# Kernel optimization log

Hardware: AMD Instinct MI355X
Metric: run time of the kernel (lower is better)

## Reference

```python
import jax, jax.numpy as jnp
import numpy as np

B, H, W = 64, 84, 84
IN_F, HID, NCLS = 128, 256, 50
C2 = IN_F * 2  # 256
EPS = 1e-5
K_NEIGH = 4


def _ring_edges(batch):
    rows = np.repeat(np.arange(batch), K_NEIGH)
    offs = np.tile(np.arange(1, K_NEIGH + 1), batch)
    cols = (rows + offs) % batch
    return jnp.asarray(np.stack([rows, cols]), dtype=jnp.int32)


def setup_inputs() -> dict:
    key = jax.random.key(0)
    ks = jax.random.split(key, 40)
    i = iter(range(40))
    def n(shape, s=0.05):
        return jax.random.normal(ks[next(i)], shape, jnp.float32) * s
    def u(shape):
        return jax.random.uniform(ks[next(i)], shape, jnp.float32, 0.5, 1.5)
    d = {}
    d['x'] = jax.random.normal(ks[next(i)], (B, 3, H, W), jnp.float32)
    # conv1 + bn1
    d['conv1_w'] = n((IN_F, 3, 3, 3)); d['conv1_b'] = n((IN_F,))
    d['bn1_g'] = 1.0 + n((IN_F,)); d['bn1_b'] = n((IN_F,))
    d['bn1_m'] = n((IN_F,)); d['bn1_v'] = u((IN_F,))
    # conv2 + bn2
    d['conv2_w'] = n((C2, IN_F, 3, 3)); d['conv2_b'] = n((C2,))
    d['bn2_g'] = 1.0 + n((C2,)); d['bn2_b'] = n((C2,))
    d['bn2_m'] = n((C2,)); d['bn2_v'] = u((C2,))
    # conv3 + bn3
    d['conv3_w'] = n((C2, C2, 3, 3)); d['conv3_b'] = n((C2,))
    d['bn3_g'] = 1.0 + n((C2,)); d['bn3_b'] = n((C2,))
    d['bn3_m'] = n((C2,)); d['bn3_v'] = u((C2,))
    # gcn1: Linear(256,256), attn Linear(512,1)
    d['gcn1_lw'] = n((HID, C2)); d['gcn1_lb'] = n((HID,))
    d['gcn1_aw'] = n((1, 2 * C2)); d['gcn1_ab'] = n((1,))
    # gcn2: Linear(256,256), attn Linear(512,1)
    d['gcn2_lw'] = n((HID, HID)); d['gcn2_lb'] = n((HID,))
    d['gcn2_aw'] = n((1, 2 * HID)); d['gcn2_ab'] = n((1,))
    # fc
    d['fc_w'] = n((NCLS, HID)); d['fc_b'] = n((NCLS,))
    d['edge_index'] = _ring_edges(B)  # [2, 4*B] deterministic ring graph
    return d


def _conv_bn_relu(x, w, b, g, be, m, v):
    y = jax.lax.conv_general_dilated(
        x, w, window_strides=(1, 1), padding='SAME',
        dimension_numbers=('NCHW', 'OIHW', 'NCHW')) + b[None, :, None, None]
    scale = (g / jnp.sqrt(v + EPS))[None, :, None, None]
    y = (y - m[None, :, None, None]) * scale + be[None, :, None, None]
    return jax.nn.relu(y)


def _gcn_conv(h, row, col, lw, lb, aw, ab):
    # h: [N, F]; edge gather -> attn MLP -> global softmax -> scatter-add
    ef = jnp.concatenate([h[row], h[col]], axis=1)          # [E, 2F]
    ew = jax.nn.leaky_relu(ef @ aw.T + ab, 0.01)            # [E, 1]
    ew = jax.nn.softmax(ew, axis=0)                          # softmax over all edges
    agg = jnp.zeros_like(h).at[row].add(h[col] * ew)        # [N, F]
    return agg @ lw.T + lb + h                               # linear + residual


def reference(x, conv1_w, conv1_b, bn1_g, bn1_b, bn1_m, bn1_v,
              conv2_w, conv2_b, bn2_g, bn2_b, bn2_m, bn2_v,
              conv3_w, conv3_b, bn3_g, bn3_b, bn3_m, bn3_v,
              gcn1_lw, gcn1_lb, gcn1_aw, gcn1_ab,
              gcn2_lw, gcn2_lb, gcn2_aw, gcn2_ab,
              fc_w, fc_b, edge_index):
    h = _conv_bn_relu(x, conv1_w, conv1_b, bn1_g, bn1_b, bn1_m, bn1_v)
    h = _conv_bn_relu(h, conv2_w, conv2_b, bn2_g, bn2_b, bn2_m, bn2_v)
    h = _conv_bn_relu(h, conv3_w, conv3_b, bn3_g, bn3_b, bn3_m, bn3_v)
    h = h.mean(axis=(2, 3))                                  # adaptive avg pool 1x1 + flatten -> [B, 256]
    row, col = edge_index[0], edge_index[1]
    h = jax.nn.relu(_gcn_conv(h, row, col, gcn1_lw, gcn1_lb, gcn1_aw, gcn1_ab))
    h = jax.nn.relu(_gcn_conv(h, row, col, gcn2_lw, gcn2_lb, gcn2_aw, gcn2_ab))
    return h @ fc_w.T + fc_b                                 # [B, 50]
```

## Files before the change

### kernel.cpp

```cpp
#include <hip/hip_runtime.h>
#include <hip/hip_bf16.h>

typedef __attribute__((ext_vector_type(8))) short bf16x8;
typedef __attribute__((ext_vector_type(4))) float f32x4;

#define DEV __device__ __forceinline__

static constexpr int Bn   = 64;
static constexpr int Hs   = 84;
static constexpr int HP   = 86;
static constexpr int C1c  = 128;
static constexpr int C2c  = 256;
static constexpr int NPOS = Hs * Hs;
static constexpr float EPSf = 1e-5f;

DEV __hip_bfloat16 f2b(float v) { return __float2bfloat16(v); }

DEV void gload16(const void* g, void* l) {
    __builtin_amdgcn_global_load_lds(
        (const __attribute__((address_space(1))) void*)g,
        (__attribute__((address_space(3))) void*)l, 16, 0, 0);
}

__global__ __launch_bounds__(128) void conv1_k(
    const float* __restrict__ x,
    const float* __restrict__ w,  const float* __restrict__ cb,
    const float* __restrict__ g,  const float* __restrict__ be,
    const float* __restrict__ mm, const float* __restrict__ vv,
    __hip_bfloat16* __restrict__ h1)
{
    __shared__ float xin[3][3][HP];
    int bi = blockIdx.x;
    int b = bi / Hs, y = bi % Hs;
    int t = threadIdx.x;

    for (int idx = t; idx < 3 * 3 * HP; idx += 128) {
        int ci = idx / (3 * HP);
        int r  = idx % (3 * HP);
        int dy = r / HP;
        int xx = r % HP;
        int iy = y + dy - 1;
        int ix = xx - 1;
        float v = 0.f;
        if (iy >= 0 && iy < Hs && ix >= 0 && ix < Hs)
            v = x[((size_t)(b * 3 + ci) * Hs + iy) * Hs + ix];
        xin[ci][dy][xx] = v;
    }
    int co = t;
    float wr[3][3][3];
    for (int ci = 0; ci < 3; ci++)
        for (int dy = 0; dy < 3; dy++)
            for (int dx = 0; dx < 3; dx++)
                wr[ci][dy][dx] = w[((co * 3 + ci) * 3 + dy) * 3 + dx];
    float scale = g[co] / sqrtf(vv[co] + EPSf);
    float bias  = (cb[co] - mm[co]) * scale + be[co];
    __syncthreads();

    for (int xp = 0; xp < Hs; xp++) {
        float acc = 0.f;
        #pragma unroll
        for (int ci = 0; ci < 3; ci++)
            #pragma unroll
            for (int dy = 0; dy < 3; dy++)
                #pragma unroll
                for (int dx = 0; dx < 3; dx++)
                    acc += xin[ci][dy][xp + dx] * wr[ci][dy][dx];
        float o = acc * scale + bias;
        o = o > 0.f ? o : 0.f;
        h1[((size_t)(b * HP + y + 1) * HP + (xp + 1)) * C1c + co] = f2b(o);
    }
}

template <int C>
__global__ void halo_zero(__hip_bfloat16* __restrict__ h)
{
    int i = blockIdx.x;
    int b = i / 340, p = i % 340;
    int y, xx;
    if (p < 86)       { y = 0;  xx = p; }
    else if (p < 172) { y = 85; xx = p - 86; }
    else if (p < 256) { xx = 0; y = p - 172 + 1; }
    else              { xx = 85; y = p - 256 + 1; }
    h[((size_t)(b * HP + y) * HP + xx) * C + threadIdx.x] = f2b(0.f);
}

template <int CIN>
__global__ void prep_w(const float* __restrict__ w, __hip_bfloat16* __restrict__ wm)
{
    int e  = blockIdx.x * 256 + threadIdx.x;
    int k  = e >> 8;
    int co = e & 255;
    int tap = k / CIN;
    int ci  = k % CIN;
    int ty = tap / 3, tx = tap % 3;
    wm[(size_t)(k >> 5) * 8192 + co * 32 + (k & 31)] =
        f2b(w[((size_t)(co * CIN + ci) * 3 + ty) * 3 + tx]);
}

__global__ void prep_sb(const float* __restrict__ cb, const float* __restrict__ g,
                        const float* __restrict__ be, const float* __restrict__ mm,
                        const float* __restrict__ vv, float* __restrict__ sb)
{
    int co = threadIdx.x;
    float s = g[co] / sqrtf(vv[co] + EPSf);
    sb[co] = s;
    sb[256 + co] = (cb[co] - mm[co]) * s + be[co];
}

__global__ void zero_f32(float* __restrict__ p)
{
    p[blockIdx.x * 256 + threadIdx.x] = 0.f;
}

template <int CIN, bool POOL>
__global__ __launch_bounds__(256) void conv_igemm(
    const __hip_bfloat16* __restrict__ in, const __hip_bfloat16* __restrict__ wm,
    const float* __restrict__ sb, __hip_bfloat16* __restrict__ out, float* __restrict__ pool)
{
    constexpr int KB = CIN / 32;
    __shared__ __align__(16) unsigned short As[128 * 32];
    __shared__ __align__(16) unsigned short Bs[128 * 32];
    __shared__ float pl[256];

    int t = threadIdx.x;
    int l = t & 63, w = t >> 6;
    int lidx = l & 15, lg = l >> 4;
    int wr = w >> 1, wc = w & 1;

    int nwg  = (int)gridDim.x;
    int orig = (int)blockIdx.x;
    int xcd = orig & 7, idx = orig >> 3;
    int q = nwg >> 3, r = nwg & 7;
    int bx = (xcd < r ? xcd * (q + 1) : r * (q + 1) + (xcd - r) * q) + idx;

    int mtile = bx >> 1, nhalf = bx & 1;
    int m0 = mtile * 128;
    int n0 = nhalf * 128;

    int srow = w * 32 + (l >> 2);
    int sseg = l & 3;
    int gmA0 = m0 + srow;
    int gmA1 = m0 + srow + 16;
    int bA0 = gmA0 / NPOS; int rA0 = gmA0 - bA0 * NPOS; int yA0 = rA0 / Hs; int xA0 = rA0 - yA0 * Hs;
    int bA1 = gmA1 / NPOS; int rA1 = gmA1 - bA1 * NPOS; int yA1 = rA1 / Hs; int xA1 = rA1 - yA1 * Hs;
    const __hip_bfloat16* aBase0 = in + ((size_t)(bA0 * HP + yA0) * HP + xA0) * CIN + sseg * 8;
    const __hip_bfloat16* aBase1 = in + ((size_t)(bA1 * HP + yA1) * HP + xA1) * CIN + sseg * 8;
    const __hip_bfloat16* bBase0 = wm + (size_t)(n0 + srow) * 32 + sseg * 8;
    const __hip_bfloat16* bBase1 = wm + (size_t)(n0 + srow + 16) * 32 + sseg * 8;
    char* aDst0 = (char*)As + (w * 32 +  0) * 64;
    char* aDst1 = (char*)As + (w * 32 + 16) * 64;
    char* bDst0 = (char*)Bs + (w * 32 +  0) * 64;
    char* bDst1 = (char*)Bs + (w * 32 + 16) * 64;

    f32x4 acc[4][4];
    #pragma unroll
    for (int i = 0; i < 4; i++)
        #pragma unroll
        for (int j = 0; j < 4; j++)
            acc[i][j] = (f32x4){0.f, 0.f, 0.f, 0.f};
    if (POOL) pl[t] = 0.f;

    for (int kb = 0; kb < KB; kb++) {
        size_t koff = (size_t)kb * 32;
        #pragma unroll
        for (int tap = 0; tap < 9; tap++) {
            int ty = tap / 3, tx = tap - ty * 3;
            size_t aoff = (size_t)(ty * HP + tx) * CIN + koff;
            size_t boff = (size_t)(tap * KB + kb) * 8192;
            gload16(aBase0 + aoff, aDst0);
            gload16(aBase1 + aoff, aDst1);
            gload16(bBase0 + boff, bDst0);
            gload16(bBase1 + boff, bDst1);
            __syncthreads();
            bf16x8 av[4], bv[4];
            #pragma unroll
            for (int m = 0; m < 4; m++)
                av[m] = *(const bf16x8*)&As[(wr * 64 + m * 16 + lidx) * 32 + lg * 8];
            #pragma unroll
            for (int n = 0; n < 4; n++)
                bv[n] = *(const bf16x8*)&Bs[(wc * 64 + n * 16 + lidx) * 32 + lg * 8];
            #pragma unroll
            for (int m = 0; m < 4; m++)
                #pragma unroll
                for (int n = 0; n < 4; n++)
                    acc[m][n] = __builtin_amdgcn_mfma_f32_16x16x32_bf16(av[m], bv[n], acc[m][n], 0, 0, 0);
            __syncthreads();
        }
    }

    float sc[4], bi2[4];
    #pragma unroll
    for (int n = 0; n < 4; n++) {
        int cn = n0 + wc * 64 + n * 16 + lidx;
        sc[n]  = sb[cn];
        bi2[n] = sb[256 + cn];
    }

    if (!POOL) {
        #pragma unroll
        for (int m = 0; m < 4; m++) {
            #pragma unroll
            for (int r2 = 0; r2 < 4; r2++) {
                int row = wr * 64 + m * 16 + lg * 4 + r2;
                int gm2 = m0 + row;
                int b2  = gm2 / NPOS;
                int rm2 = gm2 - b2 * NPOS;
                int y2  = rm2 / Hs;
                int x2  = rm2 - y2 * Hs;
                size_t ob = ((size_t)(b2 * HP + y2 + 1) * HP + (x2 + 1)) * 256;
                #pragma unroll
                for (int n = 0; n < 4; n++) {
                    float v = acc[m][n][r2] * sc[n] + bi2[n];
                    v = v > 0.f ? v : 0.f;
                    out[ob + n0 + wc * 64 + n * 16 + lidx] = f2b(v);
                }
            }
        }
    } else {
        int bs_lo   = m0 / NPOS;
        int row_lim = (bs_lo + 1) * NPOS - m0;
        #pragma unroll
        for (int n = 0; n < 4; n++) {
            float s0 = 0.f, s1 = 0.f;
            #pragma unroll
            for (int m = 0; m < 4; m++)
                #pragma unroll
                for (int r2 = 0; r2 < 4; r2++) {
                    int row = wr * 64 + m * 16 + lg * 4 + r2;
                    float v = acc[m][n][r2] * sc[n] + bi2[n];
                    v = v > 0.f ? v : 0.f;
                    if (row < row_lim) s0 += v; else s1 += v;
                }
            int cl = wc * 64 + n * 16 + lidx;
            atomicAdd(&pl[cl], s0);
            if (row_lim < 128) atomicAdd(&pl[128 + cl], s1);
        }
        __syncthreads();
        if (t < 128)
            atomicAdd(&pool[bs_lo * 256 + n0 + t], pl[t]);
        else if (row_lim < 128)
            atomicAdd(&pool[(bs_lo + 1) * 256 + n0 + (t - 128)], pl[t]);
    }
}

__global__ void pool_div(const float* __restrict__ pool, float* __restrict__ h0)
{
    int i = blockIdx.x * 256 + threadIdx.x;
    h0[i] = pool[i] * (1.0f / (float)NPOS);
}

__global__ __launch_bounds__(256) void gcn_attn(
    const float* __restrict__ h, const float* __restrict__ aw,
    const float* __restrict__ ab, const int* __restrict__ ei,
    float* __restrict__ ew)
{
    __shared__ float p[64], q[64], red[256];
    int t = threadIdx.x;
    if (t < 64) {
        float pp = 0.f, qq = 0.f;
        for (int c = 0; c < 256; c++) {
            float hv = h[t * 256 + c];
            pp += hv * aw[c];
            qq += hv * aw[256 + c];
        }
        p[t] = pp; q[t] = qq;
    }
    __syncthreads();
    int r = ei[t], c = ei[256 + t];
    float s = p[r] + q[c] + ab[0];
    s = s >= 0.f ? s : 0.01f * s;
    red[t] = s;
    __syncthreads();
    for (int st = 128; st > 0; st >>= 1) {
        if (t < st) red[t] = fmaxf(red[t], red[t + st]);
        __syncthreads();
    }
    float mx = red[0];
    __syncthreads();
    float e = expf(s - mx);
    red[t] = e;
    __syncthreads();
    for (int st = 128; st > 0; st >>= 1) {
        if (t < st) red[t] += red[t + st];
        __syncthreads();
    }
    ew[t] = e / red[0];
}

__global__ __launch_bounds__(256) void gcn_agg(
    const float* __restrict__ h, const float* __restrict__ ew, const int* __restrict__ ei,
    const float* __restrict__ lw, const float* __restrict__ lb,
    float* __restrict__ ho)
{
    __shared__ float agg[256];
    __shared__ float ewl[256];
    __shared__ int rl[256], cl[256];
    int n = blockIdx.x;
    int t = threadIdx.x;
    ewl[t] = ew[t];
    rl[t] = ei[t];
    cl[t] = ei[256 + t];
    __syncthreads();
    float a = 0.f;
    for (int e = 0; e < 256; e++)
        if (rl[e] == n) a += ewl[e] * h[cl[e] * 256 + t];
    agg[t] = a;
    __syncthreads();
    float o = 0.f;
    for (int c2 = 0; c2 < 256; c2++)
        o += agg[c2] * lw[t * 256 + c2];
    o += lb[t] + h[n * 256 + t];
    o = o > 0.f ? o : 0.f;
    ho[n * 256 + t] = o;
}

__global__ void fc_k(const float* __restrict__ h, const float* __restrict__ fw,
                     const float* __restrict__ fb, float* __restrict__ out)
{
    int n = blockIdx.x;
    int t = threadIdx.x;
    if (t < 50) {
        float o = 0.f;
        for (int c = 0; c < 256; c++)
            o += h[n * 256 + c] * fw[t * 256 + c];
        o += fb[t];
        out[n * 50 + t] = o;
    }
}

extern "C" void kernel_launch(void* const* d_in, const int* in_sizes, int n_in,
                              void* d_out, int out_size, void* d_ws, size_t ws_size,
                              hipStream_t stream)
{
    (void)in_sizes; (void)n_in; (void)out_size;

    const float* X    = (const float*)d_in[0];
    const float* c1w  = (const float*)d_in[1];
    const float* c1b  = (const float*)d_in[2];
    const float* b1g  = (const float*)d_in[3];
    const float* b1b  = (const float*)d_in[4];
    const float* b1m  = (const float*)d_in[5];
    const float* b1v  = (const float*)d_in[6];
    const float* c2w  = (const float*)d_in[7];
    const float* c2b  = (const float*)d_in[8];
    const float* b2g  = (const float*)d_in[9];
    const float* b2b  = (const float*)d_in[10];
    const float* b2m  = (const float*)d_in[11];
    const float* b2v  = (const float*)d_in[12];
    const float* c3w  = (const float*)d_in[13];
    const float* c3b  = (const float*)d_in[14];
    const float* b3g  = (const float*)d_in[15];
    const float* b3b  = (const float*)d_in[16];
    const float* b3m  = (const float*)d_in[17];
    const float* b3v  = (const float*)d_in[18];
    const float* g1lw = (const float*)d_in[19];
    const float* g1lb = (const float*)d_in[20];
    const float* g1aw = (const float*)d_in[21];
    const float* g1ab = (const float*)d_in[22];
    const float* g2lw = (const float*)d_in[23];
    const float* g2lb = (const float*)d_in[24];
    const float* g2aw = (const float*)d_in[25];
    const float* g2ab = (const float*)d_in[26];
    const float* fcw  = (const float*)d_in[27];
    const float* fcb  = (const float*)d_in[28];
    const int*   EI   = (const int*)d_in[29];

    size_t fixedB = 3000000;
    int chb = 8;
    if (ws_size >= (size_t)64 * 5680128 + fixedB)      chb = 64;
    else if (ws_size >= (size_t)32 * 5680128 + fixedB) chb = 32;
    else if (ws_size >= (size_t)16 * 5680128 + fixedB) chb = 16;
    int nchunks = Bn / chb;
    int mch = chb * NPOS;

    char* p = (char*)d_ws;
    auto carve = [&](size_t bytes) {
        char* r = p;
        p += (bytes + 255) & ~(size_t)255;
        return r;
    };
    __hip_bfloat16* h1c = (__hip_bfloat16*)carve((size_t)chb * HP * HP * C1c * 2);
    __hip_bfloat16* h2c = (__hip_bfloat16*)carve((size_t)chb * HP * HP * C2c * 2);
    __hip_bfloat16* wm2 = (__hip_bfloat16*)carve((size_t)9 * C1c * 256 * 2);
    __hip_bfloat16* wm3 = (__hip_bfloat16*)carve((size_t)9 * C2c * 256 * 2);
    float* sb2  = (float*)carve(512 * 4);
    float* sb3  = (float*)carve(512 * 4);
    float* pool = (float*)carve(64 * 256 * 4);
    float* h0   = (float*)carve(64 * 256 * 4);
    float* hg1  = (float*)carve(64 * 256 * 4);
    float* hg2  = (float*)carve(64 * 256 * 4);
    float* ew1  = (float*)carve(256 * 4);
    float* ew2  = (float*)carve(256 * 4);

    halo_zero<C1c><<<dim3(chb * 340), dim3(C1c), 0, stream>>>(h1c);
    halo_zero<C2c><<<dim3(chb * 340), dim3(C2c), 0, stream>>>(h2c);
    prep_w<C1c><<<dim3(9 * C1c), dim3(256), 0, stream>>>(c2w, wm2);
    prep_w<C2c><<<dim3(9 * C2c), dim3(256), 0, stream>>>(c3w, wm3);
    prep_sb<<<dim3(1), dim3(256), 0, stream>>>(c2b, b2g, b2b, b2m, b2v, sb2);
    prep_sb<<<dim3(1), dim3(256), 0, stream>>>(c3b, b3g, b3b, b3m, b3v, sb3);
    zero_f32<<<dim3(64), dim3(256), 0, stream>>>(pool);

    for (int ch = 0; ch < nchunks; ch++) {
        const float* xch = X + (size_t)ch * chb * 3 * NPOS;
        conv1_k<<<dim3(chb * Hs), dim3(C1c), 0, stream>>>(
            xch, c1w, c1b, b1g, b1b, b1m, b1v, h1c);
        conv_igemm<C1c, false><<<dim3((mch / 128) * 2), dim3(256), 0, stream>>>(
            h1c, wm2, sb2, h2c, nullptr);
        conv_igemm<C2c, true ><<<dim3((mch / 128) * 2), dim3(256), 0, stream>>>(
            h2c, wm3, sb3, nullptr, pool + (size_t)ch * chb * 256);
    }
    pool_div<<<dim3(64), dim3(256), 0, stream>>>(pool, h0);

    gcn_attn<<<dim3(1), dim3(256), 0, stream>>>(h0, g1aw, g1ab, EI, ew1);
    gcn_agg<<<dim3(64), dim3(256), 0, stream>>>(h0, ew1, EI, g1lw, g1lb, hg1);
    gcn_attn<<<dim3(1), dim3(256), 0, stream>>>(hg1, g2aw, g2ab, EI, ew2);
    gcn_agg<<<dim3(64), dim3(256), 0, stream>>>(hg1, ew2, EI, g2lw, g2lb, hg2);
    fc_k<<<dim3(64), dim3(64), 0, stream>>>(hg2, fcw, fcb, (float*)d_out);
}
```

Baseline: 989.3 us.

## Triple-buffer implicit-GEMM conv with full-N tiles and swizzled LDS

Reworks the conv implicit-GEMM kernel so each block computes a 128x256 output tile, covering all output channels, instead of 128x128, which halves the grid. The K loop becomes a three-stage LDS ring that issues global-to-LDS loads two steps ahead and waits with partial vmcnt, replacing the per-step double syncthreads. LDS rows get an XOR swizzle to reduce bank conflicts, and MFMA sections run with raised priority. The wider tile doubles accumulator registers and LDS use, with launch_bounds(256,2), which may limit occupancy.

```diff
diff --git a/kernel.cpp b/kernel.cpp
--- a/kernel.cpp
+++ b/kernel.cpp
@@ -113,85 +113,114 @@
 }
 
 template <int CIN, bool POOL>
-__global__ __launch_bounds__(256) void conv_igemm(
-    const __hip_bfloat16* __restrict__ in, const __hip_bfloat16* __restrict__ wm,
+__global__ __launch_bounds__(256, 2) void conv_igemm(
+    const __hip_bfloat16* __restrict__ in, const __hip_bfloat16* __restrict__ wgt,
     const float* __restrict__ sb, __hip_bfloat16* __restrict__ out, float* __restrict__ pool)
 {
     constexpr int KB = CIN / 32;
-    __shared__ __align__(16) unsigned short As[128 * 32];
-    __shared__ __align__(16) unsigned short Bs[128 * 32];
-    __shared__ float pl[256];
+    constexpr int NT = 9 * KB;
+    __shared__ __align__(16) unsigned short As[3 * 128 * 32];
+    __shared__ __align__(16) unsigned short Bs[3 * 256 * 32];
+    __shared__ float pl[512];
 
     int t = threadIdx.x;
     int l = t & 63, w = t >> 6;
     int lidx = l & 15, lg = l >> 4;
-    int wr = w >> 1, wc = w & 1;
+    int wm = w >> 1, wn = w & 1;
 
     int nwg  = (int)gridDim.x;
     int orig = (int)blockIdx.x;
     int xcd = orig & 7, idx = orig >> 3;
     int q = nwg >> 3, r = nwg & 7;
     int bx = (xcd < r ? xcd * (q + 1) : r * (q + 1) + (xcd - r) * q) + idx;
-
-    int mtile = bx >> 1, nhalf = bx & 1;
-    int m0 = mtile * 128;
-    int n0 = nhalf * 128;
-
-    int srow = w * 32 + (l >> 2);
-    int sseg = l & 3;
-    int gmA0 = m0 + srow;
-    int gmA1 = m0 + srow + 16;
-    int bA0 = gmA0 / NPOS; int rA0 = gmA0 - bA0 * NPOS; int yA0 = rA0 / Hs; int xA0 = rA0 - yA0 * Hs;
-    int bA1 = gmA1 / NPOS; int rA1 = gmA1 - bA1 * NPOS; int yA1 = rA1 / Hs; int xA1 = rA1 - yA1 * Hs;
-    const __hip_bfloat16* aBase0 = in + ((size_t)(bA0 * HP + yA0) * HP + xA0) * CIN + sseg * 8;
-    const __hip_bfloat16* aBase1 = in + ((size_t)(bA1 * HP + yA1) * HP + xA1) * CIN + sseg * 8;
-    const __hip_bfloat16* bBase0 = wm + (size_t)(n0 + srow) * 32 + sseg * 8;
-    const __hip_bfloat16* bBase1 = wm + (size_t)(n0 + srow + 16) * 32 + sseg * 8;
-    char* aDst0 = (char*)As + (w * 32 +  0) * 64;
-    char* aDst1 = (char*)As + (w * 32 + 16) * 64;
-    char* bDst0 = (char*)Bs + (w * 32 +  0) * 64;
-    char* bDst1 = (char*)Bs + (w * 32 + 16) * 64;
-
-    f32x4 acc[4][4];
+    int m0 = bx * 128;
+
+    int sseg = (l & 3) ^ ((l >> 3) & 3);
+    int srow = w * 16 + (l >> 2);
+    const __hip_bfloat16 *pA0, *pA1, *pB0, *pB1, *pB2, *pB3;
+    {
+        int gm0 = m0 + srow;
+        int b0 = gm0 / NPOS; int r0 = gm0 - b0 * NPOS; int y0 = r0 / Hs; int x0 = r0 - y0 * Hs;
+        pA0 = in + ((size_t)(b0 * HP + y0) * HP + x0) * CIN + sseg * 8;
+        int gm1 = m0 + srow + 64;
+        int b1 = gm1 / NPOS; int r1 = gm1 - b1 * NPOS; int y1 = r1 / Hs; int x1 = r1 - y1 * Hs;
+        pA1 = in + ((size_t)(b1 * HP + y1) * HP + x1) * CIN + sseg * 8;
+        pB0 = wgt + (size_t)(srow      ) * 32 + sseg * 8;
+        pB1 = wgt + (size_t)(srow +  64) * 32 + sseg * 8;
+        pB2 = wgt + (size_t)(srow + 128) * 32 + sseg * 8;
+        pB3 = wgt + (size_t)(srow + 192) * 32 + sseg * 8;
+    }
+    char* AsB = (char*)As;
+    char* BsB = (char*)Bs;
+
+    int swz = (lidx >> 1) & 3;
+    unsigned aLane = (unsigned)((wm * 64  + lidx) * 64 + ((lg ^ swz) * 16));
+    unsigned bLane = (unsigned)((wn * 128 + lidx) * 64 + ((lg ^ swz) * 16));
+
+    f32x4 acc[4][8];
     #pragma unroll
-    for (int i = 0; i < 4; i++)
-        #pragma unroll
-        for (int j = 0; j < 4; j++)
-            acc[i][j] = (f32x4){0.f, 0.f, 0.f, 0.f};
-    if (POOL) pl[t] = 0.f;
-
-    for (int kb = 0; kb < KB; kb++) {
-        size_t koff = (size_t)kb * 32;
-        #pragma unroll
-        for (int tap = 0; tap < 9; tap++) {
-            int ty = tap / 3, tx = tap - ty * 3;
-            size_t aoff = (size_t)(ty * HP + tx) * CIN + koff;
-            size_t boff = (size_t)(tap * KB + kb) * 8192;
-            gload16(aBase0 + aoff, aDst0);
-            gload16(aBase1 + aoff, aDst1);
-            gload16(bBase0 + boff, bDst0);
-            gload16(bBase1 + boff, bDst1);
-            __syncthreads();
-            bf16x8 av[4], bv[4];
+    for (int m = 0; m < 4; m++)
+        #pragma unroll
+        for (int n = 0; n < 8; n++)
+            acc[m][n] = (f32x4){0.f, 0.f, 0.f, 0.f};
+    if (POOL) { pl[t] = 0.f; pl[256 + t] = 0.f; }
+
+    auto ISSUE = [&](int k, unsigned cA, unsigned cB) {
+        int tap = k / KB, kb = k - tap * KB;
+        int ty = tap / 3, tx = tap - ty * 3;
+        size_t aoff = (size_t)(ty * HP + tx) * CIN + kb * 32;
+        size_t boff = (size_t)k * 8192;
+        gload16(pA0 + aoff, AsB + cA + w * 1024);
+        gload16(pA1 + aoff, AsB + cA + w * 1024 + 4096);
+        gload16(pB0 + boff, BsB + cB + w * 1024);
+        gload16(pB1 + boff, BsB + cB + w * 1024 + 4096);
+        gload16(pB2 + boff, BsB + cB + w * 1024 + 8192);
+        gload16(pB3 + boff, BsB + cB + w * 1024 + 12288);
+    };
+
+    auto COMP = [&](unsigned cA, unsigned cB) {
+        bf16x8 av[4]; bf16x8 bv[8];
+        #pragma unroll
+        for (int m = 0; m < 4; m++)
+            av[m] = *(const bf16x8*)(AsB + cA + aLane + m * 1024);
+        #pragma unroll
+        for (int n = 0; n < 8; n++)
+            bv[n] = *(const bf16x8*)(BsB + cB + bLane + n * 1024);
+        __builtin_amdgcn_s_setprio(1);
+        #pragma unroll
+        for (int m = 0; m < 4; m++)
             #pragma unroll
-            for (int m = 0; m < 4; m++)
-                av[m] = *(const bf16x8*)&As[(wr * 64 + m * 16 + lidx) * 32 + lg * 8];
-            #pragma unroll
-            for (int n = 0; n < 4; n++)
-                bv[n] = *(const bf16x8*)&Bs[(wc * 64 + n * 16 + lidx) * 32 + lg * 8];
-            #pragma unroll
-            for (int m = 0; m < 4; m++)
-                #pragma unroll
-                for (int n = 0; n < 4; n++)
-                    acc[m][n] = __builtin_amdgcn_mfma_f32_16x16x32_bf16(av[m], bv[n], acc[m][n], 0, 0, 0);
-            __syncthreads();
-        }
-    }
-
-    float sc[4], bi2[4];
+            for (int n = 0; n < 8; n++)
+                acc[m][n] = __builtin_amdgcn_mfma_f32_16x16x32_bf16(av[m], bv[n], acc[m][n], 0, 0, 0);
+        __builtin_amdgcn_s_setprio(0);
+    };
+
+    ISSUE(0, 0u, 0u);
+    ISSUE(1, 8192u, 16384u);
+
+    unsigned cA0 = 0u,     cB0 = 0u;
+    unsigned cA1 = 8192u,  cB1 = 16384u;
+    unsigned cA2 = 16384u, cB2 = 32768u;
+    for (int kt = 0; kt < NT - 1; ++kt) {
+        asm volatile("s_waitcnt vmcnt(6) lgkmcnt(0)" ::: "memory");
+        __builtin_amdgcn_s_barrier();
+        asm volatile("" ::: "memory");
+        if (kt + 2 < NT) ISSUE(kt + 2, cA2, cB2);
+        COMP(cA0, cB0);
+        unsigned ta = cA0, tb = cB0;
+        cA0 = cA1; cB0 = cB1;
+        cA1 = cA2; cB1 = cB2;
+        cA2 = ta;  cB2 = tb;
+    }
+    asm volatile("s_waitcnt vmcnt(0) lgkmcnt(0)" ::: "memory");
+    __builtin_amdgcn_s_barrier();
+    asm volatile("" ::: "memory");
+    COMP(cA0, cB0);
+
+    float sc[8], bi2[8];
     #pragma unroll
-    for (int n = 0; n < 4; n++) {
-        int cn = n0 + wc * 64 + n * 16 + lidx;
+    for (int n = 0; n < 8; n++) {
+        int cn = wn * 128 + n * 16 + lidx;
         sc[n]  = sb[cn];
         bi2[n] = sb[256 + cn];
     }
@@ -201,7 +230,7 @@
         for (int m = 0; m < 4; m++) {
             #pragma unroll
             for (int r2 = 0; r2 < 4; r2++) {
-                int row = wr * 64 + m * 16 + lg * 4 + r2;
+                int row = wm * 64 + m * 16 + lg * 4 + r2;
                 int gm2 = m0 + row;
                 int b2  = gm2 / NPOS;
                 int rm2 = gm2 - b2 * NPOS;
@@ -209,10 +238,10 @@
                 int x2  = rm2 - y2 * Hs;
                 size_t ob = ((size_t)(b2 * HP + y2 + 1) * HP + (x2 + 1)) * 256;
                 #pragma unroll
-                for (int n = 0; n < 4; n++) {
+                for (int n = 0; n < 8; n++) {
                     float v = acc[m][n][r2] * sc[n] + bi2[n];
                     v = v > 0.f ? v : 0.f;
-                    out[ob + n0 + wc * 64 + n * 16 + lidx] = f2b(v);
+                    out[ob + wn * 128 + n * 16 + lidx] = f2b(v);
                 }
             }
         }
@@ -220,26 +249,24 @@
         int bs_lo   = m0 / NPOS;
         int row_lim = (bs_lo + 1) * NPOS - m0;
         #pragma unroll
-        for (int n = 0; n < 4; n++) {
+        for (int n = 0; n < 8; n++) {
             float s0 = 0.f, s1 = 0.f;
             #pragma unroll
             for (int m = 0; m < 4; m++)
                 #pragma unroll
                 for (int r2 = 0; r2 < 4; r2++) {
-                    int row = wr * 64 + m * 16 + lg * 4 + r2;
+                    int row = wm * 64 + m * 16 + lg * 4 + r2;
                     float v = acc[m][n][r2] * sc[n] + bi2[n];
                     v = v > 0.f ? v : 0.f;
                     if (row < row_lim) s0 += v; else s1 += v;
                 }
-            int cl = wc * 64 + n * 16 + lidx;
+            int cl = wn * 128 + n * 16 + lidx;
             atomicAdd(&pl[cl], s0);
-            if (row_lim < 128) atomicAdd(&pl[128 + cl], s1);
+            if (row_lim < 128) atomicAdd(&pl[256 + cl], s1);
         }
         __syncthreads();
-        if (t < 128)
-            atomicAdd(&pool[bs_lo * 256 + n0 + t], pl[t]);
-        else if (row_lim < 128)
-            atomicAdd(&pool[(bs_lo + 1) * 256 + n0 + (t - 128)], pl[t]);
+        atomicAdd(&pool[bs_lo * 256 + t], pl[t]);
+        if (row_lim < 128) atomicAdd(&pool[(bs_lo + 1) * 256 + t], pl[256 + t]);
     }
 }
 
@@ -404,9 +431,9 @@
         const float* xch = X + (size_t)ch * chb * 3 * NPOS;
         conv1_k<<<dim3(chb * Hs), dim3(C1c), 0, stream>>>(
             xch, c1w, c1b, b1g, b1b, b1m, b1v, h1c);
-        conv_igemm<C1c, false><<<dim3((mch / 128) * 2), dim3(256), 0, stream>>>(
+        conv_igemm<C1c, false><<<dim3(mch / 128), dim3(256), 0, stream>>>(
             h1c, wm2, sb2, h2c, nullptr);
-        conv_igemm<C2c, true ><<<dim3((mch / 128) * 2), dim3(256), 0, stream>>>(
+        conv_igemm<C2c, true ><<<dim3(mch / 128), dim3(256), 0, stream>>>(
             h2c, wm3, sb3, nullptr, pool + (size_t)ch * chb * 256);
     }
     pool_div<<<dim3(64), dim3(256), 0, stream>>>(pool, h0);
```

Measured after the change: 1.045 ms. +5.7%, slower.

## Pipeline conv implicit-GEMM with triple-buffered LDS and a 128x256 tile

Applied to the files above, without the earlier changes.

Rewrites the conv2/conv3 implicit-GEMM main loop. Each block now has 512 threads and covers all 256 output channels for 128 pixels, which removes the duplicated A loads of the old two N-halves. Each iteration processes two K-steps, with async global-to-LDS loads issued two iterations ahead into a three-way rotating buffer. The loop uses split B fragment loads, explicit vmcnt/lgkmcnt waits, s_barrier, and setprio around the MFMA bursts. The aim is to hide global load latency and cut per-tap barrier overhead. The cost is a large LDS footprint (about 147 KB), which limits occupancy to one block per CU, plus fragile hand-written wait counts.

```diff
diff --git a/kernel.cpp b/kernel.cpp
--- a/kernel.cpp
+++ b/kernel.cpp
@@ -113,44 +113,50 @@
 }
 
 template <int CIN, bool POOL>
-__global__ __launch_bounds__(256) void conv_igemm(
-    const __hip_bfloat16* __restrict__ in, const __hip_bfloat16* __restrict__ wm,
+__global__ __launch_bounds__(512, 2) void conv_igemm(
+    const __hip_bfloat16* __restrict__ in, const __hip_bfloat16* __restrict__ wgt,
     const float* __restrict__ sb, __hip_bfloat16* __restrict__ out, float* __restrict__ pool)
 {
     constexpr int KB = CIN / 32;
-    __shared__ __align__(16) unsigned short As[128 * 32];
-    __shared__ __align__(16) unsigned short Bs[128 * 32];
-    __shared__ float pl[256];
+    constexpr int NK = 9 * KB / 2;
+    constexpr unsigned BUF = 49152u;
+    __shared__ __align__(16) char lds[3 * 49152];
+    __shared__ float pl[512];
 
     int t = threadIdx.x;
     int l = t & 63, w = t >> 6;
     int lidx = l & 15, lg = l >> 4;
-    int wr = w >> 1, wc = w & 1;
+    int wm = w >> 2, wn = w & 3;
 
     int nwg  = (int)gridDim.x;
     int orig = (int)blockIdx.x;
     int xcd = orig & 7, idx = orig >> 3;
     int q = nwg >> 3, r = nwg & 7;
     int bx = (xcd < r ? xcd * (q + 1) : r * (q + 1) + (xcd - r) * q) + idx;
-
-    int mtile = bx >> 1, nhalf = bx & 1;
-    int m0 = mtile * 128;
-    int n0 = nhalf * 128;
-
-    int srow = w * 32 + (l >> 2);
-    int sseg = l & 3;
-    int gmA0 = m0 + srow;
-    int gmA1 = m0 + srow + 16;
-    int bA0 = gmA0 / NPOS; int rA0 = gmA0 - bA0 * NPOS; int yA0 = rA0 / Hs; int xA0 = rA0 - yA0 * Hs;
-    int bA1 = gmA1 / NPOS; int rA1 = gmA1 - bA1 * NPOS; int yA1 = rA1 / Hs; int xA1 = rA1 - yA1 * Hs;
-    const __hip_bfloat16* aBase0 = in + ((size_t)(bA0 * HP + yA0) * HP + xA0) * CIN + sseg * 8;
-    const __hip_bfloat16* aBase1 = in + ((size_t)(bA1 * HP + yA1) * HP + xA1) * CIN + sseg * 8;
-    const __hip_bfloat16* bBase0 = wm + (size_t)(n0 + srow) * 32 + sseg * 8;
-    const __hip_bfloat16* bBase1 = wm + (size_t)(n0 + srow + 16) * 32 + sseg * 8;
-    char* aDst0 = (char*)As + (w * 32 +  0) * 64;
-    char* aDst1 = (char*)As + (w * 32 + 16) * 64;
-    char* bDst0 = (char*)Bs + (w * 32 +  0) * 64;
-    char* bDst1 = (char*)Bs + (w * 32 + 16) * 64;
+    int m0 = bx * 128;
+
+    int seg  = t & 3;
+    int srow = t >> 2;
+    const __hip_bfloat16* pA;
+    {
+        int gm = m0 + srow;
+        int b0 = gm / NPOS; int r0 = gm - b0 * NPOS;
+        int y0 = r0 / Hs;   int x0 = r0 - y0 * Hs;
+        pA = in + ((size_t)(b0 * HP + y0) * HP + x0) * CIN + seg * 8;
+    }
+    const __hip_bfloat16* pB = wgt + (size_t)srow * 32 + seg * 8;
+
+    unsigned aRd[4][2], bRd[4][2];
+    #pragma unroll
+    for (int mf = 0; mf < 4; mf++)
+        #pragma unroll
+        for (int kh = 0; kh < 2; kh++)
+            aRd[mf][kh] = (unsigned)(kh * 8192 + (wm * 64 + mf * 16 + lidx) * 64 + lg * 16);
+    #pragma unroll
+    for (int nf = 0; nf < 4; nf++)
+        #pragma unroll
+        for (int kh = 0; kh < 2; kh++)
+            bRd[nf][kh] = (unsigned)(16384 + kh * 16384 + (wn * 64 + nf * 16 + lidx) * 64 + lg * 16);
 
     f32x4 acc[4][4];
     #pragma unroll
@@ -160,48 +166,103 @@
             acc[i][j] = (f32x4){0.f, 0.f, 0.f, 0.f};
     if (POOL) pl[t] = 0.f;
 
-    for (int kb = 0; kb < KB; kb++) {
-        size_t koff = (size_t)kb * 32;
-        #pragma unroll
-        for (int tap = 0; tap < 9; tap++) {
-            int ty = tap / 3, tx = tap - ty * 3;
-            size_t aoff = (size_t)(ty * HP + tx) * CIN + koff;
-            size_t boff = (size_t)(tap * KB + kb) * 8192;
-            gload16(aBase0 + aoff, aDst0);
-            gload16(aBase1 + aoff, aDst1);
-            gload16(bBase0 + boff, bDst0);
-            gload16(bBase1 + boff, bDst1);
-            __syncthreads();
-            bf16x8 av[4], bv[4];
-            #pragma unroll
-            for (int m = 0; m < 4; m++)
-                av[m] = *(const bf16x8*)&As[(wr * 64 + m * 16 + lidx) * 32 + lg * 8];
-            #pragma unroll
-            for (int n = 0; n < 4; n++)
-                bv[n] = *(const bf16x8*)&Bs[(wc * 64 + n * 16 + lidx) * 32 + lg * 8];
-            #pragma unroll
-            for (int m = 0; m < 4; m++)
+    auto AOFF = [&](int s) -> size_t {
+        int kb = s / 9, tap = s - kb * 9;
+        int ty = tap / 3, tx = tap - ty * 3;
+        return (size_t)(ty * HP + tx) * CIN + kb * 32;
+    };
+    auto BOFF = [&](int s) -> size_t {
+        int kb = s / 9, tap = s - kb * 9;
+        return (size_t)(tap * KB + kb) * 8192;
+    };
+    auto ISSUE_P0 = [&](int kt2, unsigned nb) {
+        int s0 = 2 * kt2, s1 = s0 + 1;
+        gload16(pA + AOFF(s0), lds + nb +          w * 1024);
+        gload16(pA + AOFF(s1), lds + nb +  8192 + w * 1024);
+        gload16(pB + BOFF(s0), lds + nb + 16384 + w * 1024);
+    };
+    auto ISSUE_P1 = [&](int kt2, unsigned nb) {
+        int s0 = 2 * kt2, s1 = s0 + 1;
+        gload16(pB + BOFF(s0) + 4096, lds + nb + 24576 + w * 1024);
+        gload16(pB + BOFF(s1),        lds + nb + 32768 + w * 1024);
+        gload16(pB + BOFF(s1) + 4096, lds + nb + 40960 + w * 1024);
+    };
+
+    ISSUE_P0(0, 0u); ISSUE_P1(0, 0u);
+    ISSUE_P0(1, BUF); ISSUE_P1(1, BUF);
+
+    for (int kt = 0; kt < NK; ++kt) {
+        unsigned cb = (unsigned)(kt % 3) * BUF;
+        unsigned nb = (unsigned)((kt + 2) % 3) * BUF;
+        bool more = (kt + 2) < NK;
+
+        if (kt + 1 < NK) asm volatile("s_waitcnt vmcnt(6)" ::: "memory");
+        else             asm volatile("s_waitcnt vmcnt(0)" ::: "memory");
+        __builtin_amdgcn_s_barrier();
+
+        bf16x8 av[4][2], bv0[2][2];
+        #pragma unroll
+        for (int mf = 0; mf < 4; mf++)
+            #pragma unroll
+            for (int kh = 0; kh < 2; kh++)
+                av[mf][kh] = *(const bf16x8*)(lds + cb + aRd[mf][kh]);
+        #pragma unroll
+        for (int nf = 0; nf < 2; nf++)
+            #pragma unroll
+            for (int kh = 0; kh < 2; kh++)
+                bv0[nf][kh] = *(const bf16x8*)(lds + cb + bRd[nf][kh]);
+        if (more) ISSUE_P0(kt + 2, nb);
+        __builtin_amdgcn_s_barrier();
+        asm volatile("s_waitcnt lgkmcnt(0)" ::: "memory");
+        __builtin_amdgcn_sched_barrier(0);
+        __builtin_amdgcn_s_setprio(1);
+        #pragma unroll
+        for (int kh = 0; kh < 2; kh++)
+            #pragma unroll
+            for (int mf = 0; mf < 4; mf++)
                 #pragma unroll
-                for (int n = 0; n < 4; n++)
-                    acc[m][n] = __builtin_amdgcn_mfma_f32_16x16x32_bf16(av[m], bv[n], acc[m][n], 0, 0, 0);
-            __syncthreads();
-        }
+                for (int nf = 0; nf < 2; nf++)
+                    acc[mf][nf] = __builtin_amdgcn_mfma_f32_16x16x32_bf16(
+                        av[mf][kh], bv0[nf][kh], acc[mf][nf], 0, 0, 0);
+        __builtin_amdgcn_s_setprio(0);
+
+        __builtin_amdgcn_s_barrier();
+        bf16x8 bv1[2][2];
+        #pragma unroll
+        for (int nf = 0; nf < 2; nf++)
+            #pragma unroll
+            for (int kh = 0; kh < 2; kh++)
+                bv1[nf][kh] = *(const bf16x8*)(lds + cb + bRd[2 + nf][kh]);
+        if (more) ISSUE_P1(kt + 2, nb);
+        __builtin_amdgcn_s_barrier();
+        asm volatile("s_waitcnt lgkmcnt(0)" ::: "memory");
+        __builtin_amdgcn_sched_barrier(0);
+        __builtin_amdgcn_s_setprio(1);
+        #pragma unroll
+        for (int kh = 0; kh < 2; kh++)
+            #pragma unroll
+            for (int mf = 0; mf < 4; mf++)
+                #pragma unroll
+                for (int nf = 0; nf < 2; nf++)
+                    acc[mf][2 + nf] = __builtin_amdgcn_mfma_f32_16x16x32_bf16(
+                        av[mf][kh], bv1[nf][kh], acc[mf][2 + nf], 0, 0, 0);
+        __builtin_amdgcn_s_setprio(0);
     }
 
     float sc[4], bi2[4];
     #pragma unroll
-    for (int n = 0; n < 4; n++) {
-        int cn = n0 + wc * 64 + n * 16 + lidx;
-        sc[n]  = sb[cn];
-        bi2[n] = sb[256 + cn];
+    for (int nf = 0; nf < 4; nf++) {
+        int cn = wn * 64 + nf * 16 + lidx;
+        sc[nf]  = sb[cn];
+        bi2[nf] = sb[256 + cn];
     }
 
     if (!POOL) {
         #pragma unroll
-        for (int m = 0; m < 4; m++) {
+        for (int mf = 0; mf < 4; mf++) {
             #pragma unroll
             for (int r2 = 0; r2 < 4; r2++) {
-                int row = wr * 64 + m * 16 + lg * 4 + r2;
+                int row = wm * 64 + mf * 16 + lg * 4 + r2;
                 int gm2 = m0 + row;
                 int b2  = gm2 / NPOS;
                 int rm2 = gm2 - b2 * NPOS;
@@ -209,37 +270,38 @@
                 int x2  = rm2 - y2 * Hs;
                 size_t ob = ((size_t)(b2 * HP + y2 + 1) * HP + (x2 + 1)) * 256;
                 #pragma unroll
-                for (int n = 0; n < 4; n++) {
-                    float v = acc[m][n][r2] * sc[n] + bi2[n];
+                for (int nf = 0; nf < 4; nf++) {
+                    float v = acc[mf][nf][r2] * sc[nf] + bi2[nf];
                     v = v > 0.f ? v : 0.f;
-                    out[ob + n0 + wc * 64 + n * 16 + lidx] = f2b(v);
+                    out[ob + wn * 64 + nf * 16 + lidx] = f2b(v);
                 }
             }
         }
     } else {
         int bs_lo   = m0 / NPOS;
         int row_lim = (bs_lo + 1) * NPOS - m0;
-        #pragma unroll
-        for (int n = 0; n < 4; n++) {
+        __builtin_amdgcn_s_barrier();
+        #pragma unroll
+        for (int nf = 0; nf < 4; nf++) {
             float s0 = 0.f, s1 = 0.f;
             #pragma unroll
-            for (int m = 0; m < 4; m++)
+            for (int mf = 0; mf < 4; mf++)
                 #pragma unroll
                 for (int r2 = 0; r2 < 4; r2++) {
-                    int row = wr * 64 + m * 16 + lg * 4 + r2;
-                    float v = acc[m][n][r2] * sc[n] + bi2[n];
+                    int row = wm * 64 + mf * 16 + lg * 4 + r2;
+                    float v = acc[mf][nf][r2] * sc[nf] + bi2[nf];
                     v = v > 0.f ? v : 0.f;
                     if (row < row_lim) s0 += v; else s1 += v;
                 }
-            int cl = wc * 64 + n * 16 + lidx;
+            int cl = wn * 64 + nf * 16 + lidx;
             atomicAdd(&pl[cl], s0);
-            if (row_lim < 128) atomicAdd(&pl[128 + cl], s1);
+            if (row_lim < 128) atomicAdd(&pl[256 + cl], s1);
         }
         __syncthreads();
-        if (t < 128)
-            atomicAdd(&pool[bs_lo * 256 + n0 + t], pl[t]);
+        if (t < 256)
+            atomicAdd(&pool[bs_lo * 256 + t], pl[t]);
         else if (row_lim < 128)
-            atomicAdd(&pool[(bs_lo + 1) * 256 + n0 + (t - 128)], pl[t]);
+            atomicAdd(&pool[(bs_lo + 1) * 256 + (t - 256)], pl[t]);
     }
 }
 
@@ -404,9 +466,9 @@
         const float* xch = X + (size_t)ch * chb * 3 * NPOS;
         conv1_k<<<dim3(chb * Hs), dim3(C1c), 0, stream>>>(
             xch, c1w, c1b, b1g, b1b, b1m, b1v, h1c);
-        conv_igemm<C1c, false><<<dim3((mch / 128) * 2), dim3(256), 0, stream>>>(
+        conv_igemm<C1c, false><<<dim3(mch / 128), dim3(512), 0, stream>>>(
             h1c, wm2, sb2, h2c, nullptr);
-        conv_igemm<C2c, true ><<<dim3((mch / 128) * 2), dim3(256), 0, stream>>>(
+        conv_igemm<C2c, true ><<<dim3(mch / 128), dim3(512), 0, stream>>>(
             h2c, wm3, sb3, nullptr, pool + (size_t)ch * chb * 256);
     }
     pool_div<<<dim3(64), dim3(256), 0, stream>>>(pool, h0);
```

Measured after the change: 1.087 ms. 1.1x slower.
